# Performance work log

Hardware: AMD Instinct MI355X
Metric: run time of the kernel (lower is better)

The kernel has to match this reference:

```python
import jax, jax.numpy as jnp
import numpy as np
import math

B, S, D = 1, 2048, 2048
H, KVH = 16, 8
HD = D // H                      # 128
M_, N_ = 8, 256                  # S = M_*N_ blocks of tokens
FH = 5632                        # multiple_of-rounded int(2*(4*D)/3)
EPS = 1e-6
THETA = 10000.0


def rmsnorm(x, w, eps=EPS):
    xf = x.astype(jnp.float32)
    y = xf * jax.lax.rsqrt(jnp.mean(xf * xf, axis=-1, keepdims=True) + eps)
    return y.astype(x.dtype) * w


def apply_rope(x, cos, sin):
    # x: (B, S, h, HD); cos/sin: (S, HD//2) -- consecutive-pair complex rotation
    x2 = x.reshape(*x.shape[:-1], HD // 2, 2)
    xr, xi = x2[..., 0], x2[..., 1]
    c = cos[None, :, None, :]
    s = sin[None, :, None, :]
    out = jnp.stack([xr * c - xi * s, xr * s + xi * c], axis=-1)
    return out.reshape(x.shape)


def setup_inputs() -> dict:
    key = jax.random.key(0)
    ks = jax.random.split(key, 12)
    sc = 0.02
    x = jax.random.normal(ks[0], (B, S, D), jnp.float32)
    vec = jax.random.normal(ks[1], (B, M_, D), jnp.float32)
    wq = jax.random.normal(ks[2], (D, H * HD), jnp.float32) * sc
    wk = jax.random.normal(ks[3], (D, KVH * HD), jnp.float32) * sc
    wv = jax.random.normal(ks[4], (D, KVH * HD), jnp.float32) * sc
    wo = jax.random.normal(ks[5], (H * HD, D), jnp.float32) * sc
    w1 = jax.random.normal(ks[6], (D, FH), jnp.float32) * sc
    w2 = jax.random.normal(ks[7], (FH, D), jnp.float32) * sc
    w3 = jax.random.normal(ks[8], (D, FH), jnp.float32) * sc
    mod_w = jax.random.normal(ks[9], (D, 3 * D), jnp.float32) * sc
    mod_b = jnp.zeros((3 * D,), jnp.float32)
    attn_norm_w = jnp.ones((D,), jnp.float32)
    ffn_norm_w = jnp.ones((D,), jnp.float32)
    # RoPE tables
    inv = 1.0 / (THETA ** (jnp.arange(0, HD, 2, dtype=jnp.float32) / HD))
    t = jnp.arange(S, dtype=jnp.float32)
    f = jnp.outer(t, inv)                      # (S, HD//2)
    cos, sin = jnp.cos(f), jnp.sin(f)
    mask = jnp.triu(jnp.full((S, S), -1e9, jnp.float32), 1)
    return dict(x=x, vec=vec, cos=cos, sin=sin, mask=mask, wq=wq, wk=wk, wv=wv,
                wo=wo, w1=w1, w2=w2, w3=w3, mod_w=mod_w, mod_b=mod_b,
                attn_norm_w=attn_norm_w, ffn_norm_w=ffn_norm_w)


def reference(x, vec, cos, sin, mask, wq, wk, wv, wo, w1, w2, w3,
              mod_w, mod_b, attn_norm_w, ffn_norm_w):
    n_rep = H // KVH
    # Modulation from per-block vectors (B, M, D) -> expand over N tokens/block
    mod = jax.nn.silu(vec) @ mod_w + mod_b
    shift, scale, gate = jnp.split(mod, 3, axis=-1)
    expand = lambda t: jnp.repeat(t, N_, axis=1)      # (B, M, D) -> (B, S, D)
    # Attention branch with modulated RMSNorm input
    h = rmsnorm(x, attn_norm_w)
    h = (1.0 + expand(scale)) * h + expand(shift)
    q = (h @ wq).reshape(B, S, H, HD)
    k = (h @ wk).reshape(B, S, KVH, HD)
    v = (h @ wv).reshape(B, S, KVH, HD)
    q = apply_rope(q, cos, sin)
    k = apply_rope(k, cos, sin)
    k = jnp.repeat(k, n_rep, axis=2)                  # repeat_kv
    v = jnp.repeat(v, n_rep, axis=2)
    scores = jnp.einsum('bshd,bthd->bhst', q, k) / math.sqrt(HD) + mask
    attn = jax.nn.softmax(scores.astype(jnp.float32), axis=-1).astype(q.dtype)
    o = jnp.einsum('bhst,bthd->bshd', attn, v).reshape(B, S, H * HD) @ wo
    x = x + expand(gate) * o
    # SwiGLU FFN branch
    hn = rmsnorm(x, ffn_norm_w)
    ff = (jax.nn.silu(hn @ w1) * (hn @ w3)) @ w2
    return x + ff
```

## Files before the change

### kernel.cpp

```cpp
#include <hip/hip_runtime.h>
#include <hip/hip_bf16.h>


typedef __attribute__((ext_vector_type(8))) short short8;
typedef __attribute__((ext_vector_type(4))) float f32x4;
typedef __attribute__((ext_vector_type(16))) float f32x16;
typedef __attribute__((ext_vector_type(4))) unsigned short u16x4;

#define MFMA16(a, b, c) __builtin_amdgcn_mfma_f32_16x16x32_bf16((a), (b), (c), 0, 0, 0)
#define MFMA32(a, b, c) __builtin_amdgcn_mfma_f32_32x32x16_bf16((a), (b), (c), 0, 0, 0)

__device__ __forceinline__ unsigned short f2b_bits(float f) {
    union { float f; unsigned int u; } cv; cv.f = f;
    unsigned int u = cv.u;
    u += 0x7fffu + ((u >> 16) & 1u);
    return (unsigned short)(u >> 16);
}
__device__ __forceinline__ float b2f_bits(unsigned short b) {
    union { float f; unsigned int u; } cv; cv.u = ((unsigned int)b) << 16; return cv.f;
}
__device__ __forceinline__ float silu_f(float x) { return x / (1.0f + __expf(-x)); }

__device__ __forceinline__ void async_copy16(const unsigned short* g, unsigned short* l) {
    __builtin_amdgcn_global_load_lds(
        (const __attribute__((address_space(1))) unsigned int*)g,
        (__attribute__((address_space(3))) unsigned int*)l, 16, 0, 0);
}

__device__ __forceinline__ void transpose_tile(
    const float* __restrict__ W, unsigned short* __restrict__ WT,
    int K, int N, int k0, int n0, float scale, float t[64][65])
{
    const int tid = threadIdx.x;
    {
        const int row = tid >> 2, cq = (tid & 3) * 16;
        const float* src = W + (size_t)(k0 + row) * N + n0 + cq;
        #pragma unroll
        for (int i = 0; i < 4; i++) {
            float4 v = *(const float4*)(src + i * 4);
            t[row][cq + i * 4 + 0] = v.x;
            t[row][cq + i * 4 + 1] = v.y;
            t[row][cq + i * 4 + 2] = v.z;
            t[row][cq + i * 4 + 3] = v.w;
        }
    }
    __syncthreads();
    {
        const int n = tid >> 2, kq = (tid & 3) * 16;
        short8 v0, v1;
        #pragma unroll
        for (int i = 0; i < 8; i++) {
            v0[i] = (short)f2b_bits(t[kq + i][n] * scale);
            v1[i] = (short)f2b_bits(t[kq + 8 + i][n] * scale);
        }
        unsigned short* dst = WT + (size_t)(n0 + n) * K + k0 + kq;
        *(short8*)(dst) = v0;
        *(short8*)(dst + 8) = v1;
    }
}

__global__ __launch_bounds__(256) void transpose_kernel(
    const float* __restrict__ W, unsigned short* __restrict__ WT, int K, int N,
    float scale)
{
    __shared__ float t[64][65];
    transpose_tile(W, WT, K, N, blockIdx.y * 64, blockIdx.x * 64, scale, t);
}

__global__ __launch_bounds__(256) void transpose_qkv_kernel(
    const float* __restrict__ wq, const float* __restrict__ wk,
    const float* __restrict__ wv, unsigned short* __restrict__ WTqkv,
    float qscale)
{
    __shared__ float t[64][65];
    const int x = blockIdx.x, k0 = blockIdx.y * 64;
    if (x < 32) {
        transpose_tile(wq, WTqkv, 2048, 2048, k0, x * 64, qscale, t);
    } else if (x < 48) {
        transpose_tile(wk, WTqkv + (size_t)2048 * 2048, 2048, 1024, k0, (x - 32) * 64, 1.0f, t);
    } else {
        transpose_tile(wv, WTqkv + (size_t)3072 * 2048, 2048, 1024, k0, (x - 48) * 64, 1.0f, t);
    }
}

__global__ __launch_bounds__(256) void transpose_w13_kernel(
    const float* __restrict__ w1, const float* __restrict__ w3,
    unsigned short* __restrict__ WT1, unsigned short* __restrict__ WT3)
{
    __shared__ float t[64][65];
    const float* W = blockIdx.z ? w3 : w1;
    unsigned short* WT = blockIdx.z ? WT3 : WT1;
    transpose_tile(W, WT, 2048, 5632, blockIdx.y * 64, blockIdx.x * 64, 1.0f, t);
}

__global__ __launch_bounds__(256) void mod_gemm1(
    const float* __restrict__ vec, const float* __restrict__ mw,
    float* __restrict__ part)
{
    __shared__ float svs[8][256];
    const int tid = threadIdx.x;
    const int nb = blockIdx.x, kc = blockIdx.y;
    const int n = nb * 256 + tid;
    #pragma unroll
    for (int m8 = 0; m8 < 8; m8++) svs[m8][tid] = silu_f(vec[m8 * 2048 + kc * 256 + tid]);
    __syncthreads();
    float acc[8];
    #pragma unroll
    for (int m = 0; m < 8; m++) acc[m] = 0.0f;
    for (int k = 0; k < 256; k++) {
        const float w = mw[(size_t)(kc * 256 + k) * 6144 + n];
        #pragma unroll
        for (int m = 0; m < 8; m++) acc[m] += svs[m][k] * w;
    }
    #pragma unroll
    for (int m = 0; m < 8; m++) part[(size_t)(kc * 8 + m) * 6144 + n] = acc[m];
}

__global__ void mod_gemm2(const float* __restrict__ part, const float* __restrict__ mb,
                          float* __restrict__ modb)
{
    const int i = blockIdx.x * 256 + threadIdx.x;
    const int n = i % 6144;
    float a = mb[n];
    #pragma unroll
    for (int kc = 0; kc < 8; kc++) a += part[(size_t)(kc * 8 + (i / 6144)) * 6144 + n];
    modb[i] = a;
}

__global__ __launch_bounds__(256) void norm_mod_kernel(
    const float* __restrict__ xin, const float* __restrict__ w,
    const float* __restrict__ mod, unsigned short* __restrict__ outp)
{
    const int s = blockIdx.x, tid = threadIdx.x;
    const float* xr = xin + (size_t)s * 2048;
    float4 a4 = *(const float4*)(xr + tid * 8);
    float4 b4 = *(const float4*)(xr + tid * 8 + 4);
    float v[8] = {a4.x, a4.y, a4.z, a4.w, b4.x, b4.y, b4.z, b4.w};
    float ss = 0.0f;
    #pragma unroll
    for (int i = 0; i < 8; i++) ss += v[i] * v[i];
    #pragma unroll
    for (int off = 1; off < 64; off <<= 1) ss += __shfl_xor(ss, off);
    __shared__ float red[4];
    if ((tid & 63) == 0) red[tid >> 6] = ss;
    __syncthreads();
    ss = red[0] + red[1] + red[2] + red[3];
    const float inv = rsqrtf(ss * (1.0f / 2048.0f) + 1e-6f);
    const int g = s >> 8;
    #pragma unroll
    for (int i = 0; i < 8; i++) {
        const int d = tid * 8 + i;
        float y = v[i] * inv * w[d];
        y = y * (1.0f + mod[g * 6144 + 2048 + d]) + mod[g * 6144 + d];
        outp[(size_t)s * 2048 + d] = f2b_bits(y);
    }
}

__global__ __launch_bounds__(256) void combine_norm_kernel(
    const float* __restrict__ p, const float* __restrict__ x,
    const float* __restrict__ modp, const float* __restrict__ fnw,
    float* __restrict__ out, unsigned short* __restrict__ hn)
{
    const int s = blockIdx.x, tid = threadIdx.x;
    const int g = s >> 8;
    const size_t base = (size_t)s * 2048 + tid * 8;
    float v[8];
    #pragma unroll
    for (int i = 0; i < 8; i += 4) {
        const float4 a  = *(const float4*)(p + base + i);
        const float4 b  = *(const float4*)(p + (size_t)2048 * 2048 + base + i);
        const float4 xv = *(const float4*)(x + base + i);
        const float4 gv = *(const float4*)(modp + g * 6144 + 4096 + tid * 8 + i);
        v[i + 0] = xv.x + gv.x * (a.x + b.x);
        v[i + 1] = xv.y + gv.y * (a.y + b.y);
        v[i + 2] = xv.z + gv.z * (a.z + b.z);
        v[i + 3] = xv.w + gv.w * (a.w + b.w);
    }
    *(float4*)(out + base)     = (float4){v[0], v[1], v[2], v[3]};
    *(float4*)(out + base + 4) = (float4){v[4], v[5], v[6], v[7]};
    float ss = 0.0f;
    #pragma unroll
    for (int i = 0; i < 8; i++) ss += v[i] * v[i];
    #pragma unroll
    for (int off = 1; off < 64; off <<= 1) ss += __shfl_xor(ss, off);
    __shared__ float red[4];
    if ((tid & 63) == 0) red[tid >> 6] = ss;
    __syncthreads();
    ss = red[0] + red[1] + red[2] + red[3];
    const float inv = rsqrtf(ss * (1.0f / 2048.0f) + 1e-6f);
    #pragma unroll
    for (int i = 0; i < 8; i++) {
        const int d = tid * 8 + i;
        hn[(size_t)s * 2048 + d] = f2b_bits(v[i] * inv * fnw[d]);
    }
}

enum { EP_QKV = 0, EP_BF16 = 1, EP_SILUMUL = 2, EP_PART = 3 };

template<int EPI>
__global__ __launch_bounds__(256, 2) void gemm_kernel(
    const unsigned short* __restrict__ A, const unsigned short* __restrict__ BT,
    void* __restrict__ outp, void* __restrict__ outp2, void* __restrict__ outp3,
    const unsigned short* __restrict__ up,
    const float* __restrict__ ct, const float* __restrict__ st,
    int M, int N, int K, int kspl)
{
    __shared__ unsigned short As[8192];
    __shared__ unsigned short Bs[8192];
    const int tid = threadIdx.x;
    const int lane = tid & 63, wave = tid >> 6;

    const int nwg = gridDim.x * gridDim.y;
    const int fid = blockIdx.y * gridDim.x + blockIdx.x;
    const int sid = (fid & 7) * (nwg >> 3) + (fid >> 3);
    const int m0 = (sid / gridDim.x) * 128;
    const int n0 = (sid % gridDim.x) * 128;
    const int kb0 = blockIdx.z * kspl;

    const int wr = (wave >> 1) * 64, wc = (wave & 1) * 64;
    const int lr = lane & 15, lg = lane >> 4;
    const int rcol = (lg ^ ((lr >> 1) & 3)) * 8;

    const int cl0 = (wave * 2 + 0) * 64 + lane;
    const int cl1 = (wave * 2 + 1) * 64 + lane;
    const int r0 = cl0 >> 2, c0 = cl0 & 3;
    const int r1 = cl1 >> 2, c1 = cl1 & 3;
    const unsigned short* gA0 = A + (size_t)(m0 + r0) * K + kb0 + (c0 ^ ((r0 >> 1) & 3)) * 8;
    const unsigned short* gA1 = A + (size_t)(m0 + r1) * K + kb0 + (c1 ^ ((r1 >> 1) & 3)) * 8;
    const unsigned short* gB0 = BT + (size_t)(n0 + r0) * K + kb0 + (c0 ^ ((r0 >> 1) & 3)) * 8;
    const unsigned short* gB1 = BT + (size_t)(n0 + r1) * K + kb0 + (c1 ^ ((r1 >> 1) & 3)) * 8;

    f32x4 acc[4][4];
    #pragma unroll
    for (int i = 0; i < 4; i++)
        #pragma unroll
        for (int j = 0; j < 4; j++) acc[i][j] = (f32x4){0.f, 0.f, 0.f, 0.f};

    const int nsteps = kspl >> 5;

    auto stage = [&](int buf, int kofs) {
        unsigned short* la = As + buf * 4096 + wave * 1024;
        unsigned short* lb = Bs + buf * 4096 + wave * 1024;
        async_copy16(gA0 + kofs, la);
        async_copy16(gA1 + kofs, la + 512);
        async_copy16(gB0 + kofs, lb);
        async_copy16(gB1 + kofs, lb + 512);
    };
    auto dostep = [&](int t, int cur) {
        if (t + 1 < nsteps) stage(cur ^ 1, (t + 1) * 32);
        const unsigned short* ab = As + cur * 4096;
        const unsigned short* bb = Bs + cur * 4096;
        short8 af[4], bfr[4];
        #pragma unroll
        for (int i = 0; i < 4; i++)
            af[i] = *(const short8*)&ab[(wr + i * 16 + lr) * 32 + rcol];
        #pragma unroll
        for (int j = 0; j < 4; j++)
            bfr[j] = *(const short8*)&bb[(wc + j * 16 + lr) * 32 + rcol];
        #pragma unroll
        for (int i = 0; i < 4; i++)
            #pragma unroll
            for (int j = 0; j < 4; j++)
                acc[i][j] = MFMA16(af[i], bfr[j], acc[i][j]);
        __syncthreads();
    };

    stage(0, 0);
    __syncthreads();
    for (int t = 0; t < nsteps; t += 2) { dostep(t, 0); dostep(t + 1, 1); }

    #pragma unroll
    for (int i = 0; i < 4; i++) {
        #pragma unroll
        for (int j = 0; j < 4; j++) {
            const int rb = m0 + wr + i * 16 + lg * 4;
            const int c  = n0 + wc + j * 16 + lr;
            if constexpr (EPI == EP_QKV) {
                if (n0 < 3072) {
                    const int crel = (n0 < 2048) ? c : (c - 2048);
                    const int dd = crel & 127;
                    const int pr = dd >> 1;
                    #pragma unroll
                    for (int r = 0; r < 4; r++) {
                        const float v = acc[i][j][r];
                        const float p = __shfl_xor(v, 1);
                        const float cs = ct[(rb + r) * 64 + pr];
                        const float sn = st[(rb + r) * 64 + pr];
                        const float res = (dd & 1) ? (p * sn + v * cs) : (v * cs - p * sn);
                        if (n0 < 2048)
                            ((unsigned short*)outp)[(size_t)(rb + r) * 2048 + crel] = f2b_bits(res);
                        else
                            ((unsigned short*)outp2)[(size_t)(rb + r) * 1024 + crel] = f2b_bits(res);
                    }
                } else {
                    u16x4 pk4;
                    #pragma unroll
                    for (int r = 0; r < 4; r++) pk4[r] = f2b_bits(acc[i][j][r]);
                    *(u16x4*)((unsigned short*)outp3 + (size_t)(c - 3072) * 2048 + rb) = pk4;
                }
            } else if constexpr (EPI == EP_PART) {
                float* pout = (float*)outp + (size_t)blockIdx.z * M * N;
                #pragma unroll
                for (int r = 0; r < 4; r++)
                    pout[(size_t)(rb + r) * N + c] = acc[i][j][r];
            } else {
                #pragma unroll
                for (int r = 0; r < 4; r++) {
                    const size_t idx = (size_t)(rb + r) * N + c;
                    if constexpr (EPI == EP_BF16) {
                        ((unsigned short*)outp)[idx] = f2b_bits(acc[i][j][r]);
                    } else {
                        const float uu = b2f_bits(up[idx]);
                        ((unsigned short*)outp)[idx] = f2b_bits(silu_f(uu) * acc[i][j][r]);
                    }
                }
            }
        }
    }
}

__global__ void combine_w2(const float* __restrict__ p, float* __restrict__ out)
{
    const size_t i = ((size_t)blockIdx.x * 256 + threadIdx.x) * 4;
    const float4 a = *(const float4*)(p + i);
    const float4 b = *(const float4*)(p + (size_t)2048 * 2048 + i);
    float4 o = *(const float4*)(out + i);
    o.x += a.x + b.x; o.y += a.y + b.y; o.z += a.z + b.z; o.w += a.w + b.w;
    *(float4*)(out + i) = o;
}

__global__ __launch_bounds__(256, 2) void attn_kernel(
    const unsigned short* __restrict__ q,
    const unsigned short* __restrict__ kk,
    const unsigned short* __restrict__ vT,
    unsigned short* __restrict__ o)
{
    __shared__ unsigned short Ks[2][8192];
    __shared__ unsigned short Vs[2][8192];
    const int tid = threadIdx.x, wave = tid >> 6, lane = tid & 63;
    const int l5 = lane & 31, hi = lane >> 5;
    const int kvh = blockIdx.x;
    const int qt  = 63 - blockIdx.y;
    const int hs = wave >> 1, ks = wave & 1;
    const int h = kvh * 2 + hs;
    const int q0 = qt * 32;
    const int qrow = q0 + l5;
    const int niter = (qt >> 1) + 1;
    const int nss = (niter + 1) >> 1;

    short8 qf[8];
    {
        const unsigned short* qp = q + (size_t)qrow * 2048 + h * 128 + hi * 8;
        #pragma unroll
        for (int kf = 0; kf < 8; kf++) qf[kf] = *(const short8*)(qp + kf * 16);
    }

    f32x16 ot[4];
    #pragma unroll
    for (int df = 0; df < 4; df++)
        #pragma unroll
        for (int r = 0; r < 16; r++) ot[df][r] = 0.0f;
    float m_ = -3e30f, l_ = 0.0f;

    for (int ss = 0; ss < nss; ss++) {
        const int kvA = ss * 128;
        #pragma unroll
        for (int t = 0; t < 2; t++) {
            #pragma unroll
            for (int i = 0; i < 4; i++) {
                const int cl = (wave * 4 + i) * 64 + lane;
                const int row = cl >> 4, c = cl & 15;
                async_copy16(kk + (size_t)(kvA + t * 64 + row) * 1024 + kvh * 128
                                 + ((c ^ (row & 15)) * 8),
                             &Ks[t][(wave * 4 + i) * 512]);
            }
            #pragma unroll
            for (int i = 0; i < 4; i++) {
                const int cl = (wave * 4 + i) * 64 + lane;
                const int row = cl >> 3, c = cl & 7;
                async_copy16(vT + (size_t)(kvh * 128 + row) * 2048 + kvA + t * 64
                                 + ((c ^ (row & 7)) * 8),
                             &Vs[t][(wave * 4 + i) * 512]);
            }
        }
        __syncthreads();

        const int j = 2 * ss + ks;
        if (j < niter) {
            const int kv0 = j * 64;
            f32x16 st_[2];
            #pragma unroll
            for (int nf = 0; nf < 2; nf++)
                #pragma unroll
                for (int r = 0; r < 16; r++) st_[nf][r] = 0.0f;
            #pragma unroll
            for (int kf = 0; kf < 8; kf++) {
                const int ch = (kf * 2 + hi) ^ (l5 & 15);
                const short8 k0v = *(const short8*)&Ks[ks][l5 * 128 + ch * 8];
                const short8 k1v = *(const short8*)&Ks[ks][(l5 + 32) * 128 + ch * 8];
                st_[0] = MFMA32(k0v, qf[kf], st_[0]);
                st_[1] = MFMA32(k1v, qf[kf], st_[1]);
            }
            float sv[2][16];
            #pragma unroll
            for (int nf = 0; nf < 2; nf++)
                #pragma unroll
                for (int r = 0; r < 16; r++) {
                    const int kvi = kv0 + nf * 32 + (r & 3) + 8 * (r >> 2) + 4 * hi;
                    sv[nf][r] = (kvi > qrow) ? -3e30f : st_[nf][r];
                }
            float pmax = sv[0][0];
            #pragma unroll
            for (int nf = 0; nf < 2; nf++)
                #pragma unroll
                for (int r = 0; r < 16; r++) pmax = fmaxf(pmax, sv[nf][r]);
            pmax = fmaxf(pmax, __shfl_xor(pmax, 32));
            const float mnew = fmaxf(m_, pmax);
            const float alpha = __expf(m_ - mnew);
            m_ = mnew;
            float rs = 0.0f;
            #pragma unroll
            for (int nf = 0; nf < 2; nf++)
                #pragma unroll
                for (int r = 0; r < 16; r++) {
                    const float p = __expf(sv[nf][r] - mnew);
                    sv[nf][r] = p;
                    rs += p;
                }
            rs += __shfl_xor(rs, 32);
            l_ = l_ * alpha + rs;
            #pragma unroll
            for (int df = 0; df < 4; df++)
                #pragma unroll
                for (int r = 0; r < 16; r++) ot[df][r] *= alpha;
            short8 pa[4];
            #pragma unroll
            for (int nf = 0; nf < 2; nf++) {
                #pragma unroll
                for (int hh = 0; hh < 2; hh++) {
                    unsigned int a0 = ((unsigned int)f2b_bits(sv[nf][8 * hh + 1]) << 16) | f2b_bits(sv[nf][8 * hh + 0]);
                    unsigned int a1 = ((unsigned int)f2b_bits(sv[nf][8 * hh + 3]) << 16) | f2b_bits(sv[nf][8 * hh + 2]);
                    unsigned int a2 = ((unsigned int)f2b_bits(sv[nf][8 * hh + 5]) << 16) | f2b_bits(sv[nf][8 * hh + 4]);
                    unsigned int a3 = ((unsigned int)f2b_bits(sv[nf][8 * hh + 7]) << 16) | f2b_bits(sv[nf][8 * hh + 6]);
                    const unsigned int x0 = (unsigned int)__shfl_xor((int)a0, 32);
                    const unsigned int x1 = (unsigned int)__shfl_xor((int)a1, 32);
                    const unsigned int x2 = (unsigned int)__shfl_xor((int)a2, 32);
                    const unsigned int x3 = (unsigned int)__shfl_xor((int)a3, 32);
                    union { unsigned int u[4]; short8 s; } cv;
                    cv.u[0] = hi ? x2 : a0;
                    cv.u[1] = hi ? x3 : a1;
                    cv.u[2] = hi ? a2 : x0;
                    cv.u[3] = hi ? a3 : x1;
                    pa[nf * 2 + hh] = cv.s;
                }
            }
            #pragma unroll
            for (int df = 0; df < 4; df++) {
                const int d = df * 32 + l5;
                #pragma unroll
                for (int kvf = 0; kvf < 4; kvf++) {
                    const int ch = (kvf * 2 + hi) ^ (d & 7);
                    const short8 vfrag = *(const short8*)&Vs[ks][d * 64 + ch * 8];
                    ot[df] = MFMA32(vfrag, pa[kvf], ot[df]);
                }
            }
        }
        __syncthreads();
    }

    float* Osh = (float*)&Ks[0][0];
    float* msh = (float*)&Vs[0][0];
    if (ks == 1) {
        #pragma unroll
        for (int df = 0; df < 4; df++)
            #pragma unroll
            for (int r = 0; r < 16; r++) {
                const int d = df * 32 + (r & 3) + 8 * (r >> 2) + 4 * hi;
                Osh[hs * 4096 + d * 32 + l5] = ot[df][r];
            }
        if (hi == 0) { msh[hs * 64 + l5] = m_; msh[hs * 64 + 32 + l5] = l_; }
    }
    __syncthreads();
    if (ks == 0) {
        const float m1 = msh[hs * 64 + l5], l1 = msh[hs * 64 + 32 + l5];
        const float mF = fmaxf(m_, m1);
        const float a0 = __expf(m_ - mF), a1 = __expf(m1 - mF);
        const float rinv = 1.0f / (l_ * a0 + l1 * a1);
        #pragma unroll
        for (int df = 0; df < 4; df++) {
            #pragma unroll
            for (int g = 0; g < 4; g++) {
                u16x4 pk;
                #pragma unroll
                for (int e = 0; e < 4; e++) {
                    const int d = df * 32 + e + 8 * g + 4 * hi;
                    const float ov = ot[df][4 * g + e] * a0 + Osh[hs * 4096 + d * 32 + l5] * a1;
                    pk[e] = f2b_bits(ov * rinv);
                }
                *(u16x4*)(o + (size_t)qrow * 2048 + h * 128 + df * 32 + 8 * g + 4 * hi) = pk;
            }
        }
    }
}

extern "C" void kernel_launch(void* const* d_in, const int* in_sizes, int n_in,
                              void* d_out, int out_size, void* d_ws, size_t ws_size,
                              hipStream_t stream) {
    (void)in_sizes; (void)n_in; (void)out_size; (void)ws_size;
    const float* x     = (const float*)d_in[0];
    const float* vec   = (const float*)d_in[1];
    const float* cosb  = (const float*)d_in[2];
    const float* sinb  = (const float*)d_in[3];
    const float* wq    = (const float*)d_in[5];
    const float* wk    = (const float*)d_in[6];
    const float* wv    = (const float*)d_in[7];
    const float* wo    = (const float*)d_in[8];
    const float* w1    = (const float*)d_in[9];
    const float* w2    = (const float*)d_in[10];
    const float* w3    = (const float*)d_in[11];
    const float* mod_w = (const float*)d_in[12];
    const float* mod_b = (const float*)d_in[13];
    const float* anw   = (const float*)d_in[14];
    const float* fnw   = (const float*)d_in[15];
    float* out = (float*)d_out;

    char* ws = (char*)d_ws;
    size_t off = 0;
    auto alloc = [&](size_t bytes) -> void* {
        void* p = ws + off; off += (bytes + 255) & ~(size_t)255; return p;
    };
    unsigned short* WTqkv = (unsigned short*)alloc((size_t)4096 * 2048 * 2);
    unsigned short* WTo   = (unsigned short*)alloc((size_t)2048 * 2048 * 2);
    unsigned short* WT1   = (unsigned short*)alloc((size_t)5632 * 2048 * 2);
    unsigned short* WT3   = (unsigned short*)alloc((size_t)5632 * 2048 * 2);
    unsigned short* WT2   = (unsigned short*)alloc((size_t)2048 * 5632 * 2);
    float* part = (float*)alloc((size_t)64 * 6144 * 4);
    float* modb = (float*)alloc((size_t)8 * 6144 * 4);
    unsigned short* h    = (unsigned short*)alloc((size_t)2048 * 2048 * 2);
    unsigned short* qb   = (unsigned short*)alloc((size_t)2048 * 2048 * 2);
    unsigned short* kb   = (unsigned short*)alloc((size_t)2048 * 1024 * 2);
    unsigned short* vT   = (unsigned short*)alloc((size_t)1024 * 2048 * 2);
    unsigned short* ob   = (unsigned short*)alloc((size_t)2048 * 2048 * 2);
    unsigned short* u    = (unsigned short*)alloc((size_t)2048 * 5632 * 2);
    unsigned short* ffin = (unsigned short*)alloc((size_t)2048 * 5632 * 2);

    float* pxg = (float*)u;
    float* pw2 = (float*)h;

    const float qscale = 0.08838834764831845f;

    transpose_qkv_kernel<<<dim3(64, 32), 256, 0, stream>>>(wq, wk, wv, WTqkv, qscale);
    transpose_kernel<<<dim3(32, 32), 256, 0, stream>>>(wo, WTo, 2048, 2048, 1.0f);
    transpose_w13_kernel<<<dim3(88, 32, 2), 256, 0, stream>>>(w1, w3, WT1, WT3);
    transpose_kernel<<<dim3(32, 88), 256, 0, stream>>>(w2, WT2, 5632, 2048, 1.0f);

    mod_gemm1<<<dim3(24, 8), 256, 0, stream>>>(vec, mod_w, part);
    mod_gemm2<<<192, 256, 0, stream>>>(part, mod_b, modb);

    norm_mod_kernel<<<2048, 256, 0, stream>>>(x, anw, modb, h);

    gemm_kernel<EP_QKV><<<dim3(32, 16), 256, 0, stream>>>(
        h, WTqkv, qb, kb, vT, nullptr, cosb, sinb, 2048, 4096, 2048, 2048);

    attn_kernel<<<dim3(8, 64), 256, 0, stream>>>(qb, kb, vT, ob);

    gemm_kernel<EP_PART><<<dim3(16, 16, 2), 256, 0, stream>>>(
        ob, WTo, pxg, nullptr, nullptr, nullptr, nullptr, nullptr, 2048, 2048, 2048, 1024);
    combine_norm_kernel<<<2048, 256, 0, stream>>>(pxg, x, modb, fnw, out, h);

    gemm_kernel<EP_BF16><<<dim3(44, 16), 256, 0, stream>>>(
        h, WT1, u, nullptr, nullptr, nullptr, nullptr, nullptr, 2048, 5632, 2048, 2048);
    gemm_kernel<EP_SILUMUL><<<dim3(44, 16), 256, 0, stream>>>(
        h, WT3, ffin, nullptr, nullptr, u, nullptr, nullptr, 2048, 5632, 2048, 2048);

    gemm_kernel<EP_PART><<<dim3(16, 16, 2), 256, 0, stream>>>(
        ffin, WT2, pw2, nullptr, nullptr, nullptr, nullptr, nullptr, 2048, 2048, 5632, 2816);
    combine_w2<<<4096, 256, 0, stream>>>(pw2, out);
}
```

Baseline: 445.9 us.

## Restructure attention blocks to 64-row query slabs with double-buffered KV pipeline

Each attention block now handles a 64-row query slab: its four waves cover two heads times two 32-row query halves over the full KV range, replacing the old split of the KV range across waves with a final cross-wave merge. KV tiles are loaded one 64-token tile at a time with double buffering, so the next tile's load overlaps current compute, and the merge through shared memory is removed. The grid is halved to 256 blocks, so each K/V tile is loaded once and shared by more query rows. The cost is less parallelism and longer per-block serial loops for the late slabs, which may hurt load balance.

```diff
diff --git a/kernel.cpp b/kernel.cpp
--- a/kernel.cpp
+++ b/kernel.cpp
@@ -340,13 +340,11 @@
     const int tid = threadIdx.x, wave = tid >> 6, lane = tid & 63;
     const int l5 = lane & 31, hi = lane >> 5;
     const int kvh = blockIdx.x;
-    const int qt  = 63 - blockIdx.y;
-    const int hs = wave >> 1, ks = wave & 1;
+    const int slab = 31 - blockIdx.y;
+    const int hs = wave >> 1, qs = wave & 1;
     const int h = kvh * 2 + hs;
-    const int q0 = qt * 32;
-    const int qrow = q0 + l5;
-    const int niter = (qt >> 1) + 1;
-    const int nss = (niter + 1) >> 1;
+    const int qrow = slab * 64 + qs * 32 + l5;
+    const int ntiles = slab + 1;
 
     short8 qf[8];
     {
@@ -362,143 +360,121 @@
         for (int r = 0; r < 16; r++) ot[df][r] = 0.0f;
     float m_ = -3e30f, l_ = 0.0f;
 
-    for (int ss = 0; ss < nss; ss++) {
-        const int kvA = ss * 128;
-        #pragma unroll
-        for (int t = 0; t < 2; t++) {
-            #pragma unroll
-            for (int i = 0; i < 4; i++) {
-                const int cl = (wave * 4 + i) * 64 + lane;
-                const int row = cl >> 4, c = cl & 15;
-                async_copy16(kk + (size_t)(kvA + t * 64 + row) * 1024 + kvh * 128
-                                 + ((c ^ (row & 15)) * 8),
-                             &Ks[t][(wave * 4 + i) * 512]);
+    auto stage = [&](int j, int b) {
+        #pragma unroll
+        for (int i = 0; i < 4; i++) {
+            const int cl = (wave * 4 + i) * 64 + lane;
+            const int row = cl >> 4, c = cl & 15;
+            async_copy16(kk + (size_t)(j * 64 + row) * 1024 + kvh * 128
+                             + ((c ^ (row & 15)) * 8),
+                         &Ks[b][(wave * 4 + i) * 512]);
+        }
+        #pragma unroll
+        for (int i = 0; i < 4; i++) {
+            const int cl = (wave * 4 + i) * 64 + lane;
+            const int row = cl >> 3, c = cl & 7;
+            async_copy16(vT + (size_t)(kvh * 128 + row) * 2048 + j * 64
+                             + ((c ^ (row & 7)) * 8),
+                         &Vs[b][(wave * 4 + i) * 512]);
+        }
+    };
+
+    stage(0, 0);
+    __syncthreads();
+
+    for (int j = 0; j < ntiles; ++j) {
+        const int buf = j & 1;
+        if (j + 1 < ntiles) stage(j + 1, buf ^ 1);
+        const int kv0 = j * 64;
+        f32x16 st_[2];
+        #pragma unroll
+        for (int nf = 0; nf < 2; nf++)
+            #pragma unroll
+            for (int r = 0; r < 16; r++) st_[nf][r] = 0.0f;
+        #pragma unroll
+        for (int kf = 0; kf < 8; kf++) {
+            const int ch = (kf * 2 + hi) ^ (l5 & 15);
+            const short8 k0v = *(const short8*)&Ks[buf][l5 * 128 + ch * 8];
+            const short8 k1v = *(const short8*)&Ks[buf][(l5 + 32) * 128 + ch * 8];
+            st_[0] = MFMA32(k0v, qf[kf], st_[0]);
+            st_[1] = MFMA32(k1v, qf[kf], st_[1]);
+        }
+        float sv[2][16];
+        #pragma unroll
+        for (int nf = 0; nf < 2; nf++)
+            #pragma unroll
+            for (int r = 0; r < 16; r++) {
+                const int kvi = kv0 + nf * 32 + (r & 3) + 8 * (r >> 2) + 4 * hi;
+                sv[nf][r] = (kvi > qrow) ? -3e30f : st_[nf][r];
             }
-            #pragma unroll
-            for (int i = 0; i < 4; i++) {
-                const int cl = (wave * 4 + i) * 64 + lane;
-                const int row = cl >> 3, c = cl & 7;
-                async_copy16(vT + (size_t)(kvh * 128 + row) * 2048 + kvA + t * 64
-                                 + ((c ^ (row & 7)) * 8),
-                             &Vs[t][(wave * 4 + i) * 512]);
+        float pmax = sv[0][0];
+        #pragma unroll
+        for (int nf = 0; nf < 2; nf++)
+            #pragma unroll
+            for (int r = 0; r < 16; r++) pmax = fmaxf(pmax, sv[nf][r]);
+        pmax = fmaxf(pmax, __shfl_xor(pmax, 32));
+        const float mnew = fmaxf(m_, pmax);
+        const float alpha = __expf(m_ - mnew);
+        m_ = mnew;
+        float rs = 0.0f;
+        #pragma unroll
+        for (int nf = 0; nf < 2; nf++)
+            #pragma unroll
+            for (int r = 0; r < 16; r++) {
+                const float p = __expf(sv[nf][r] - mnew);
+                sv[nf][r] = p;
+                rs += p;
             }
+        rs += __shfl_xor(rs, 32);
+        l_ = l_ * alpha + rs;
+        #pragma unroll
+        for (int df = 0; df < 4; df++)
+            #pragma unroll
+            for (int r = 0; r < 16; r++) ot[df][r] *= alpha;
+        short8 pa[4];
+        #pragma unroll
+        for (int nf = 0; nf < 2; nf++) {
+            #pragma unroll
+            for (int hh = 0; hh < 2; hh++) {
+                unsigned int a0 = ((unsigned int)f2b_bits(sv[nf][8 * hh + 1]) << 16) | f2b_bits(sv[nf][8 * hh + 0]);
+                unsigned int a1 = ((unsigned int)f2b_bits(sv[nf][8 * hh + 3]) << 16) | f2b_bits(sv[nf][8 * hh + 2]);
+                unsigned int a2 = ((unsigned int)f2b_bits(sv[nf][8 * hh + 5]) << 16) | f2b_bits(sv[nf][8 * hh + 4]);
+                unsigned int a3 = ((unsigned int)f2b_bits(sv[nf][8 * hh + 7]) << 16) | f2b_bits(sv[nf][8 * hh + 6]);
+                const unsigned int x0 = (unsigned int)__shfl_xor((int)a0, 32);
+                const unsigned int x1 = (unsigned int)__shfl_xor((int)a1, 32);
+                const unsigned int x2 = (unsigned int)__shfl_xor((int)a2, 32);
+                const unsigned int x3 = (unsigned int)__shfl_xor((int)a3, 32);
+                union { unsigned int u[4]; short8 s; } cv;
+                cv.u[0] = hi ? x2 : a0;
+                cv.u[1] = hi ? x3 : a1;
+                cv.u[2] = hi ? a2 : x0;
+                cv.u[3] = hi ? a3 : x1;
+                pa[nf * 2 + hh] = cv.s;
+            }
+        }
+        #pragma unroll
+        for (int df = 0; df < 4; df++) {
+            const int d = df * 32 + l5;
+            #pragma unroll
+            for (int kvf = 0; kvf < 4; kvf++) {
+                const int ch = (kvf * 2 + hi) ^ (d & 7);
+                const short8 vfrag = *(const short8*)&Vs[buf][d * 64 + ch * 8];
+                ot[df] = MFMA32(vfrag, pa[kvf], ot[df]);
+            }
         }
         __syncthreads();
-
-        const int j = 2 * ss + ks;
-        if (j < niter) {
-            const int kv0 = j * 64;
-            f32x16 st_[2];
-            #pragma unroll
-            for (int nf = 0; nf < 2; nf++)
-                #pragma unroll
-                for (int r = 0; r < 16; r++) st_[nf][r] = 0.0f;
-            #pragma unroll
-            for (int kf = 0; kf < 8; kf++) {
-                const int ch = (kf * 2 + hi) ^ (l5 & 15);
-                const short8 k0v = *(const short8*)&Ks[ks][l5 * 128 + ch * 8];
-                const short8 k1v = *(const short8*)&Ks[ks][(l5 + 32) * 128 + ch * 8];
-                st_[0] = MFMA32(k0v, qf[kf], st_[0]);
-                st_[1] = MFMA32(k1v, qf[kf], st_[1]);
-            }
-            float sv[2][16];
-            #pragma unroll
-            for (int nf = 0; nf < 2; nf++)
-                #pragma unroll
-                for (int r = 0; r < 16; r++) {
-                    const int kvi = kv0 + nf * 32 + (r & 3) + 8 * (r >> 2) + 4 * hi;
-                    sv[nf][r] = (kvi > qrow) ? -3e30f : st_[nf][r];
-                }
-            float pmax = sv[0][0];
-            #pragma unroll
-            for (int nf = 0; nf < 2; nf++)
-                #pragma unroll
-                for (int r = 0; r < 16; r++) pmax = fmaxf(pmax, sv[nf][r]);
-            pmax = fmaxf(pmax, __shfl_xor(pmax, 32));
-            const float mnew = fmaxf(m_, pmax);
-            const float alpha = __expf(m_ - mnew);
-            m_ = mnew;
-            float rs = 0.0f;
-            #pragma unroll
-            for (int nf = 0; nf < 2; nf++)
-                #pragma unroll
-                for (int r = 0; r < 16; r++) {
-                    const float p = __expf(sv[nf][r] - mnew);
-                    sv[nf][r] = p;
-                    rs += p;
-                }
-            rs += __shfl_xor(rs, 32);
-            l_ = l_ * alpha + rs;
-            #pragma unroll
-            for (int df = 0; df < 4; df++)
-                #pragma unroll
-                for (int r = 0; r < 16; r++) ot[df][r] *= alpha;
-            short8 pa[4];
-            #pragma unroll
-            for (int nf = 0; nf < 2; nf++) {
-                #pragma unroll
-                for (int hh = 0; hh < 2; hh++) {
-                    unsigned int a0 = ((unsigned int)f2b_bits(sv[nf][8 * hh + 1]) << 16) | f2b_bits(sv[nf][8 * hh + 0]);
-                    unsigned int a1 = ((unsigned int)f2b_bits(sv[nf][8 * hh + 3]) << 16) | f2b_bits(sv[nf][8 * hh + 2]);
-                    unsigned int a2 = ((unsigned int)f2b_bits(sv[nf][8 * hh + 5]) << 16) | f2b_bits(sv[nf][8 * hh + 4]);
-                    unsigned int a3 = ((unsigned int)f2b_bits(sv[nf][8 * hh + 7]) << 16) | f2b_bits(sv[nf][8 * hh + 6]);
-                    const unsigned int x0 = (unsigned int)__shfl_xor((int)a0, 32);
-                    const unsigned int x1 = (unsigned int)__shfl_xor((int)a1, 32);
-                    const unsigned int x2 = (unsigned int)__shfl_xor((int)a2, 32);
-                    const unsigned int x3 = (unsigned int)__shfl_xor((int)a3, 32);
-                    union { unsigned int u[4]; short8 s; } cv;
-                    cv.u[0] = hi ? x2 : a0;
-                    cv.u[1] = hi ? x3 : a1;
-                    cv.u[2] = hi ? a2 : x0;
-                    cv.u[3] = hi ? a3 : x1;
-                    pa[nf * 2 + hh] = cv.s;
-                }
-            }
-            #pragma unroll
-            for (int df = 0; df < 4; df++) {
-                const int d = df * 32 + l5;
-                #pragma unroll
-                for (int kvf = 0; kvf < 4; kvf++) {
-                    const int ch = (kvf * 2 + hi) ^ (d & 7);
-                    const short8 vfrag = *(const short8*)&Vs[ks][d * 64 + ch * 8];
-                    ot[df] = MFMA32(vfrag, pa[kvf], ot[df]);
-                }
-            }
-        }
-        __syncthreads();
-    }
-
-    float* Osh = (float*)&Ks[0][0];
-    float* msh = (float*)&Vs[0][0];
-    if (ks == 1) {
-        #pragma unroll
-        for (int df = 0; df < 4; df++)
-            #pragma unroll
-            for (int r = 0; r < 16; r++) {
-                const int d = df * 32 + (r & 3) + 8 * (r >> 2) + 4 * hi;
-                Osh[hs * 4096 + d * 32 + l5] = ot[df][r];
-            }
-        if (hi == 0) { msh[hs * 64 + l5] = m_; msh[hs * 64 + 32 + l5] = l_; }
-    }
-    __syncthreads();
-    if (ks == 0) {
-        const float m1 = msh[hs * 64 + l5], l1 = msh[hs * 64 + 32 + l5];
-        const float mF = fmaxf(m_, m1);
-        const float a0 = __expf(m_ - mF), a1 = __expf(m1 - mF);
-        const float rinv = 1.0f / (l_ * a0 + l1 * a1);
-        #pragma unroll
-        for (int df = 0; df < 4; df++) {
-            #pragma unroll
-            for (int g = 0; g < 4; g++) {
-                u16x4 pk;
-                #pragma unroll
-                for (int e = 0; e < 4; e++) {
-                    const int d = df * 32 + e + 8 * g + 4 * hi;
-                    const float ov = ot[df][4 * g + e] * a0 + Osh[hs * 4096 + d * 32 + l5] * a1;
-                    pk[e] = f2b_bits(ov * rinv);
-                }
-                *(u16x4*)(o + (size_t)qrow * 2048 + h * 128 + df * 32 + 8 * g + 4 * hi) = pk;
-            }
+    }
+
+    const float rinv = 1.0f / l_;
+    #pragma unroll
+    for (int df = 0; df < 4; df++) {
+        #pragma unroll
+        for (int g = 0; g < 4; g++) {
+            u16x4 pk;
+            #pragma unroll
+            for (int e = 0; e < 4; e++)
+                pk[e] = f2b_bits(ot[df][4 * g + e] * rinv);
+            *(u16x4*)(o + (size_t)qrow * 2048 + h * 128 + df * 32 + 8 * g + 4 * hi) = pk;
         }
     }
 }
@@ -562,7 +538,7 @@
     gemm_kernel<EP_QKV><<<dim3(32, 16), 256, 0, stream>>>(
         h, WTqkv, qb, kb, vT, nullptr, cosb, sinb, 2048, 4096, 2048, 2048);
 
-    attn_kernel<<<dim3(8, 64), 256, 0, stream>>>(qb, kb, vT, ob);
+    attn_kernel<<<dim3(8, 32), 256, 0, stream>>>(qb, kb, vT, ob);
 
     gemm_kernel<EP_PART><<<dim3(16, 16, 2), 256, 0, stream>>>(
         ob, WTo, pxg, nullptr, nullptr, nullptr, nullptr, nullptr, 2048, 2048, 2048, 1024);
```

After: 475.5 us. +6.6%, slower.
